# Kernel optimization log

Hardware: AMD Instinct MI355X
Metric: run time of the kernel (lower is better)

Reference implementation:

```python
import jax, jax.numpy as jnp
import numpy as np

K = 5            # dimW
PARAM_SIGMA = 0.08
LAMBDA_V = 2.0
C_MID = 192


def _conv5(x, w, b):
    # standard 5x5 SAME conv (the linear 'm' term of INRF)
    y = jax.lax.conv_general_dilated(x, w, (1, 1), 'SAME',
                                     dimension_numbers=('NCHW', 'OIHW', 'NCHW'))
    return y + b[None, :, None, None]


def _inrf(x, m_w, m_b, w_w):
    """INRF layer: out = (m * x) - lambda * sum_y w(y) sigma(x(y) - (g*x)(center)).
    dimG=1 so the Gaussian g*x is the identity (center pixel). The radiometric
    nonlinearity sigma is a saturating tanh with slope 1/paramSigma.
    """
    B, C, H, W = x.shape
    # windowed gather: [B, C*K*K, H, W], channel-major / spatial-minor ordering
    patches = jax.lax.conv_general_dilated_patches(x, (K, K), (1, 1), 'SAME')
    patches = patches.reshape(B, C, K * K, H, W)
    s = jnp.tanh((patches - x[:, :, None]) / PARAM_SIGMA)   # [B,C,KK,H,W]
    wterm = jnp.einsum('bckhw,ock->bohw', s, w_w)           # [B,Cout,H,W]
    return _conv5(x, m_w, m_b) - LAMBDA_V * wterm


def _maxpool2(x):
    return jax.lax.reduce_window(x, -jnp.inf, jax.lax.max,
                                 (1, 1, 2, 2), (1, 1, 2, 2), 'VALID')


def _avgpool8(x):
    s = jax.lax.reduce_window(x, 0.0, jax.lax.add,
                              (1, 1, 8, 8), (1, 1, 8, 8), 'VALID')
    return s / 64.0


def setup_inputs() -> dict:
    key = jax.random.key(0)
    ks = jax.random.split(key, 11)
    B = 64
    f32 = jnp.float32
    return {
        'x':    jax.random.normal(ks[0], (B, 3, 32, 32), f32),
        'm1_w': jax.random.normal(ks[1], (C_MID, 3, K, K), f32) * 0.05,
        'm1_b': jnp.zeros((C_MID,), f32),
        'w1_w': jax.random.normal(ks[2], (C_MID, 3, K * K), f32) * 0.05,
        'm2_w': jax.random.normal(ks[3], (C_MID, C_MID, K, K), f32) * 0.02,
        'm2_b': jnp.zeros((C_MID,), f32),
        'w2_w': jax.random.normal(ks[4], (C_MID, C_MID, K * K), f32) * 0.02,
        'm3_w': jax.random.normal(ks[5], (C_MID, C_MID, K, K), f32) * 0.02,
        'm3_b': jnp.zeros((C_MID,), f32),
        'w3_w': jax.random.normal(ks[6], (C_MID, C_MID, K * K), f32) * 0.02,
        'fc_w': jax.random.normal(ks[7], (10, C_MID), f32) * 0.05,
        'fc_b': jnp.zeros((10,), f32),
    }


def reference(x, m1_w, m1_b, w1_w, m2_w, m2_b, w2_w,
              m3_w, m3_b, w3_w, fc_w, fc_b):
    # dropout layers run in eval mode (identity); dp2d1 has p=0.0 anyway
    x00 = _maxpool2(_inrf(x, m1_w, m1_b, w1_w))      # [B,192,16,16]
    x01 = _inrf(x00, m2_w, m2_b, w2_w)               # [B,192,16,16]
    x03 = _maxpool2(x01)                             # [B,192,8,8]
    x04 = _inrf(x03, m3_w, m3_b, w3_w)               # [B,192,8,8]
    x05 = _avgpool8(x04)                             # [B,192,1,1]
    feat = x05.reshape(-1, C_MID)
    logits = feat @ fc_w.T + fc_b                    # [B,10]
    return (logits, x00, x01)
```

## Files before the change

kernel.cpp:

```cpp
#include <hip/hip_runtime.h>
#include <math.h>

#define COUT 192
#define NF 12

typedef __bf16 bf16_8 __attribute__((ext_vector_type(8)));
typedef float  f32x4  __attribute__((ext_vector_type(4)));

__device__ __forceinline__ float fast_tanh125(float d) {
    float e = __builtin_amdgcn_exp2f(d * 36.06737602222409f);
    return 1.0f - 2.0f * __builtin_amdgcn_rcpf(e + 1.0f);
}

__device__ __forceinline__ void gl_lds16(const void* gptr, void* lptr) {
    auto g = (const __attribute__((address_space(1))) unsigned int*)gptr;
    auto l = (__attribute__((address_space(3))) unsigned int*)lptr;
    __builtin_amdgcn_global_load_lds(g, l, 16, 0, 0);
}

__global__ void prep_all(const float* __restrict__ m1_w, const float* __restrict__ w1_w,
                         const float* __restrict__ m2_w, const float* __restrict__ w2_w,
                         const float* __restrict__ m3_w, const float* __restrict__ w3_w,
                         __bf16* __restrict__ Bp1, __bf16* __restrict__ Bp2,
                         __bf16* __restrict__ Bp3, float* __restrict__ x00p) {
    int idx = blockIdx.x * 256 + threadIdx.x;
    const int N1 = 3 * 2 * NF * 64, N2 = 192 * 2 * NF * 64;
    const int NW = N1 + 2 * N2;
    if (idx >= NW) {
        int zi = idx - NW;
        if (zi < 1228800) ((f32x4*)x00p)[zi] = (f32x4){0.f, 0.f, 0.f, 0.f};
        return;
    }
    const float *mw, *ww; __bf16* Bp; int CIN, li;
    if (idx < N1)           { mw = m1_w; ww = w1_w; Bp = Bp1; CIN = 3;   li = idx; }
    else if (idx < N1 + N2) { mw = m2_w; ww = w2_w; Bp = Bp2; CIN = 192; li = idx - N1; }
    else                    { mw = m3_w; ww = w3_w; Bp = Bp3; CIN = 192; li = idx - N1 - N2; }
    int lane = li & 63;
    int nf = (li >> 6) % NF;
    int cc = li / (NF * 64);
    int t = cc & 1, c = cc >> 1;
    int n = nf * 16 + (lane & 15);
    int k0 = (lane >> 4) * 8;
    bf16_8 v;
    #pragma unroll
    for (int e = 0; e < 8; ++e) {
        int k = k0 + e;
        float val = 0.f;
        if (k < 25) {
            val = (t == 0) ? mw[((size_t)n * CIN + c) * 25 + k]
                           : -2.0f * ww[((size_t)n * CIN + c) * 25 + k];
        }
        v[e] = (__bf16)val;
    }
    *(bf16_8*)(Bp + (size_t)li * 8) = v;
}

__global__ __launch_bounds__(256, 3) void inrf1_mfma(
    const float* __restrict__ x, const __bf16* __restrict__ Bp,
    const float* __restrict__ bias, float* __restrict__ x00,
    float* __restrict__ x00p)
{
    __shared__ float win[3][6][36];
    __shared__ float hp[192][33];

    const int b  = blockIdx.x >> 4;
    const int h0 = (blockIdx.x & 15) * 2;
    const int tid = threadIdx.x;
    const int wv = tid >> 6, lane = tid & 63;
    const int hl = wv >> 1, half = wv & 1;
    const int mcol = lane & 15, q = lane >> 4;
    const int wpos = half * 16 + mcol;

    for (int i = tid; i < 3 * 6 * 36; i += 256) {
        int c = i / 216, r = (i / 36) % 6, cc = i % 36;
        int gr = h0 + r - 2, gc = cc - 2;
        float v = 0.f;
        if (gr >= 0 && gr < 32 && gc >= 0 && gc < 32)
            v = x[((size_t)(b * 3 + c) * 32 + gr) * 32 + gc];
        win[c][r][cc] = v;
    }
    __syncthreads();

    int offs[8];
    #pragma unroll
    for (int e = 0; e < 8; ++e) {
        int k = q * 8 + e;
        int kk = (k < 25) ? k : 0;
        offs[e] = (hl + kk / 5) * 36 + wpos + (kk % 5);
    }
    const int cen_off = (hl + 2) * 36 + wpos + 2;

    f32x4 acc[NF];
    #pragma unroll
    for (int j = 0; j < NF; ++j) acc[j] = (f32x4){0.f, 0.f, 0.f, 0.f};

    const float* winf = &win[0][0][0];
    for (int c = 0; c < 3; ++c) {
        const float* wf = winf + c * 216;
        float cen = wf[cen_off];
        bf16_8 av, as_;
        #pragma unroll
        for (int e = 0; e < 8; ++e) {
            float v = wf[offs[e]];
            av[e] = (__bf16)v;
            as_[e] = (__bf16)fast_tanh125(v - cen);
        }
        const bf16_8* b0 = (const bf16_8*)Bp + ((size_t)(c * 2 + 0) * NF) * 64 + lane;
        const bf16_8* b1 = b0 + NF * 64;
        #pragma unroll
        for (int j = 0; j < NF; ++j)
            acc[j] = __builtin_amdgcn_mfma_f32_16x16x32_bf16(av, b0[j * 64], acc[j], 0, 0, 0);
        #pragma unroll
        for (int j = 0; j < NF; ++j)
            acc[j] = __builtin_amdgcn_mfma_f32_16x16x32_bf16(as_, b1[j * 64], acc[j], 0, 0, 0);
    }

    #pragma unroll
    for (int j = 0; j < NF; ++j) {
        int n = j * 16 + mcol;
        hp[n][hl * 16 + half * 8 + q * 2 + 0] = fmaxf(acc[j][0], acc[j][1]);
        hp[n][hl * 16 + half * 8 + q * 2 + 1] = fmaxf(acc[j][2], acc[j][3]);
    }
    __syncthreads();

    const int hpout = h0 >> 1;
    for (int i = tid; i < 192 * 16; i += 256) {
        int n = i >> 4, wp = i & 15;
        float v = fmaxf(hp[n][wp], hp[n][16 + wp]) + bias[n];
        x00[((size_t)(b * COUT + n) * 16 + hpout) * 16 + wp] = v;
        x00p[(size_t)(b * COUT + n) * 400 + (hpout + 2) * 20 + (wp + 2)] = v;
    }
}

__global__ __launch_bounds__(512, 2) void inrf2_mfma(
    const float* __restrict__ x00p, const __bf16* __restrict__ Bp,
    float* __restrict__ out0, float* __restrict__ part)
{
    constexpr int CPS = 48;
    __shared__ __align__(16) __bf16 Bs[3][24 * 64 * 8];

    const int b  = blockIdx.x >> 2;
    const int ks = blockIdx.x & 3;
    const int c0 = ks * CPS;
    const int tid = threadIdx.x;
    const int wv = tid >> 6, lane = tid & 63;
    const int mg = wv & 3, nh = wv >> 2;
    const int wp = lane & 15, q = lane >> 4;

    int goff[9];
    #pragma unroll
    for (int e = 0; e < 8; ++e) {
        int kk = q * 8 + e;
        int k2 = (kk < 25) ? kk : 12;
        int dy = k2 / 5 - 2, dx = k2 % 5 - 2;
        goff[e] = (mg * 4 + dy + 2) * 20 + (wp + dx + 2);
    }
    goff[8] = (mg * 4 + 2) * 20 + (wp + 2);

    const float* xs = x00p + (size_t)(b * COUT + c0) * 400;

    f32x4 acc[4][6];
    #pragma unroll
    for (int m = 0; m < 4; ++m)
        #pragma unroll
        for (int j = 0; j < 6; ++j) acc[m][j] = (f32x4){0.f, 0.f, 0.f, 0.f};

#define ISSUE_B(c, slot)                                                   \
    {                                                                      \
        const __bf16* gB = Bp + (size_t)(c) * 12288 + wv * 1536 + lane * 8;\
        _Pragma("unroll")                                                  \
        for (int i = 0; i < 3; ++i)                                        \
            gl_lds16(gB + i * 512, &Bs[(slot)][wv * 1536 + i * 512]);      \
    }

#define LOAD_A(c, DST)                                                     \
    {                                                                      \
        const float* xc = xs + (size_t)(c) * 400;                          \
        _Pragma("unroll")                                                  \
        for (int m = 0; m < 4; ++m) {                                      \
            _Pragma("unroll")                                              \
            for (int i = 0; i < 9; ++i)                                    \
                (DST)[m][i] = xc[goff[i] + m * 20];                        \
        }                                                                  \
    }

#define STEP(r, CUR, NXT)                                                  \
    {                                                                      \
        const int sl_cur = (r) % 3;                                        \
        if ((r) + 2 < CPS) ISSUE_B(c0 + (r) + 2, ((r) + 2) % 3);           \
        if ((r) + 1 < CPS) LOAD_A((r) + 1, NXT);                           \
        bf16_8 av[4], as_[4];                                              \
        _Pragma("unroll")                                                  \
        for (int m = 0; m < 4; ++m) {                                      \
            float cen = (CUR)[m][8];                                       \
            _Pragma("unroll")                                              \
            for (int e = 0; e < 8; ++e) {                                  \
                float v = (CUR)[m][e];                                     \
                av[m][e] = (__bf16)v;                                      \
                as_[m][e] = (__bf16)fast_tanh125(v - cen);                 \
            }                                                              \
        }                                                                  \
        const bf16_8* Bf = (const bf16_8*)(Bs[sl_cur]) + lane;             \
        _Pragma("unroll")                                                  \
        for (int j = 0; j < 6; ++j) {                                      \
            bf16_8 fm = Bf[(nh * 6 + j) * 64];                             \
            bf16_8 fs = Bf[(12 + nh * 6 + j) * 64];                        \
            _Pragma("unroll")                                              \
            for (int m = 0; m < 4; ++m) {                                  \
                acc[m][j] = __builtin_amdgcn_mfma_f32_16x16x32_bf16(av[m],  fm, acc[m][j], 0, 0, 0); \
                acc[m][j] = __builtin_amdgcn_mfma_f32_16x16x32_bf16(as_[m], fs, acc[m][j], 0, 0, 0); \
            }                                                              \
        }                                                                  \
        __builtin_amdgcn_s_barrier();                                      \
    }

    float arawA[4][9], arawB[4][9];

    ISSUE_B(c0, 0);
    asm volatile("s_waitcnt vmcnt(0)" ::: "memory");
    __builtin_amdgcn_s_barrier();
    ISSUE_B(c0 + 1, 1);
    LOAD_A(0, arawA);

    for (int r2 = 0; r2 < CPS / 2; ++r2) {
        STEP(2 * r2,     arawA, arawB);
        STEP(2 * r2 + 1, arawB, arawA);
    }
#undef STEP
#undef LOAD_A
#undef ISSUE_B

    float* outp = (ks == 0) ? out0 : (part + (size_t)(ks - 1) * 3145728);
    #pragma unroll
    for (int j = 0; j < 6; ++j) {
        int n = (nh * 6 + j) * 16 + wp;
        #pragma unroll
        for (int m = 0; m < 4; ++m) {
            int h = mg * 4 + m;
            *(f32x4*)&outp[((size_t)(b * COUT + n)) * 256 + h * 16 + q * 4] = acc[m][j];
        }
    }
}

__global__ __launch_bounds__(512) void finish2(
    float* __restrict__ x01, const float* __restrict__ part,
    const float* __restrict__ bias, __bf16* __restrict__ An)
{
    __shared__ float xbuf[8][256];
    const int b  = blockIdx.x / 24;
    const int cg = blockIdx.x % 24;
    const int tid = threadIdx.x;
    const int wv = tid >> 6, lane = tid & 63;
    const int ch = cg * 8 + wv;

    float* p0 = x01 + ((size_t)b * COUT + ch) * 256;
    const float* pp = part + ((size_t)b * COUT + ch) * 256;
    const float bv = bias[ch];
    #pragma unroll
    for (int i = 0; i < 4; ++i) {
        int idx = lane + 64 * i;
        float s = ((p0[idx] + pp[idx]) + pp[idx + 3145728]) + pp[idx + 2 * 3145728] + bv;
        xbuf[wv][idx] = s;
        p0[idx] = s;
    }
    __syncthreads();

    const int ph = lane >> 3, pw = lane & 7;
    const int i0 = ph * 32 + pw * 2;
    float x8 = fmaxf(fmaxf(xbuf[wv][i0], xbuf[wv][i0 + 1]),
                     fmaxf(xbuf[wv][i0 + 16], xbuf[wv][i0 + 17]));

    float myT = 0.f, myW = 0.f;
    #pragma unroll
    for (int k = 0; k < 25; ++k) {
        const int dy = k / 5 - 2, dx = k % 5 - 2;
        const bool valid = (ph + dy >= 0) && (ph + dy < 8) && (pw + dx >= 0) && (pw + dx < 8);
        float nb = __shfl(x8, (lane + dy * 8 + dx) & 63);
        nb = valid ? nb : 0.f;
        float tS = fast_tanh125(nb - x8);
        float wS = nb;
        #pragma unroll
        for (int off = 1; off < 64; off <<= 1) {
            tS += __shfl_xor(tS, off);
            wS += __shfl_xor(wS, off);
        }
        if (lane == k) { myT = tS; myW = wS; }
    }

    const int mt = b >> 4;
    if (lane < 25) {
        const int k = lane;
        const int la = (k >> 3) * 16 + (b & 15);
        const int e = k & 7;
        const int ccW = ch * 2, ccT = ch * 2 + 1;
        An[((size_t)(ccW * 4 + mt) * 64 + la) * 8 + e] = (__bf16)(myW * 0.015625f);
        An[((size_t)(ccT * 4 + mt) * 64 + la) * 8 + e] = (__bf16)(myT * 0.015625f);
    } else if (lane < 32) {
        const int la = 3 * 16 + (b & 15);
        const int e = lane & 7;
        const int ccW = ch * 2, ccT = ch * 2 + 1;
        An[((size_t)(ccW * 4 + mt) * 64 + la) * 8 + e] = (__bf16)0.f;
        An[((size_t)(ccT * 4 + mt) * 64 + la) * 8 + e] = (__bf16)0.f;
    }
}

__global__ __launch_bounds__(512) void gemm3p(
    const __bf16* __restrict__ An, const __bf16* __restrict__ Bp,
    float* __restrict__ part)
{
    const int ks = blockIdx.x;
    const int tid = threadIdx.x;
    const int wv = tid >> 6, lane = tid & 63;
    const int mt = wv & 3, nh = wv >> 2;

    f32x4 acc[6];
    #pragma unroll
    for (int j = 0; j < 6; ++j) acc[j] = (f32x4){0.f, 0.f, 0.f, 0.f};

    for (int i = 0; i < 4; ++i) {
        const int cc = ks * 4 + i;
        bf16_8 a = *(const bf16_8*)(An + ((size_t)(cc * 4 + mt) * 64 + lane) * 8);
        #pragma unroll
        for (int j = 0; j < 6; ++j) {
            bf16_8 bw = *(const bf16_8*)(Bp + ((size_t)(cc * NF + nh * 6 + j) * 64 + lane) * 8);
            acc[j] = __builtin_amdgcn_mfma_f32_16x16x32_bf16(a, bw, acc[j], 0, 0, 0);
        }
    }
    #pragma unroll
    for (int j = 0; j < 6; ++j) {
        int n = (nh * 6 + j) * 16 + (lane & 15);
        *(f32x4*)(part + ((size_t)ks * COUT + n) * 64 + mt * 16 + (lane >> 4) * 4) = acc[j];
    }
}

__global__ __launch_bounds__(256) void logitsk(
    const float* __restrict__ part, const float* __restrict__ m3_b,
    const float* __restrict__ fc_w, const float* __restrict__ fc_b,
    float* __restrict__ logits)
{
    __shared__ float feat[COUT];
    const int b = blockIdx.x;
    const int t = threadIdx.x;
    if (t < COUT) {
        float s = 0.f;
        for (int ks = 0; ks < 96; ++ks) s += part[((size_t)ks * COUT + t) * 64 + b];
        feat[t] = s + m3_b[t];
    }
    __syncthreads();
    if (t < 10) {
        float s = fc_b[t];
        #pragma unroll 8
        for (int c = 0; c < COUT; ++c) s = fmaf(fc_w[t * COUT + c], feat[c], s);
        logits[(size_t)b * 10 + t] = s;
    }
}

extern "C" void kernel_launch(void* const* d_in, const int* in_sizes, int n_in,
                              void* d_out, int out_size, void* d_ws, size_t ws_size,
                              hipStream_t stream) {
    const float* x    = (const float*)d_in[0];
    const float* m1_w = (const float*)d_in[1];
    const float* m1_b = (const float*)d_in[2];
    const float* w1_w = (const float*)d_in[3];
    const float* m2_w = (const float*)d_in[4];
    const float* m2_b = (const float*)d_in[5];
    const float* w2_w = (const float*)d_in[6];
    const float* m3_w = (const float*)d_in[7];
    const float* m3_b = (const float*)d_in[8];
    const float* w3_w = (const float*)d_in[9];
    const float* fc_w = (const float*)d_in[10];
    const float* fc_b = (const float*)d_in[11];

    float* out = (float*)d_out;
    float* ws  = (float*)d_ws;

    float* logits = out;
    float* x00 = out + 640;
    float* x01 = out + 640 + 3145728;

    __bf16* Bp1  = (__bf16*)(ws);
    __bf16* Bp2  = (__bf16*)(ws + 18432);
    __bf16* Bp3  = (__bf16*)(ws + 1198080);
    __bf16* An   = (__bf16*)(ws + 2377728);
    float*  part2 = ws + 2770944;
    float*  part3 = ws + 2770944;
    float*  x00p  = ws + 12208128;

    prep_all<<<7122, 256, 0, stream>>>(m1_w, w1_w, m2_w, w2_w, m3_w, w3_w,
                                       Bp1, Bp2, Bp3, x00p);

    inrf1_mfma<<<64 * 16, 256, 0, stream>>>(x, Bp1, m1_b, x00, x00p);
    inrf2_mfma<<<64 * 4, 512, 0, stream>>>(x00p, Bp2, x01, part2);
    finish2<<<64 * 24, 512, 0, stream>>>(x01, part2, m2_b, An);
    gemm3p<<<96, 512, 0, stream>>>(An, Bp3, part3);
    logitsk<<<64, 256, 0, stream>>>(part3, m3_b, fc_w, fc_b, logits);
}
```

Baseline: 231.0 us.

## Load inrf2 weights directly into registers and split output channels across blocks

The inrf2 kernel stops staging B weight fragments through LDS with global_load_lds and barriers. Each wave now loads its weight fragments straight into registers with double buffering, while the A-side patch loads move inline into each step. The grid doubles to 512 blocks of 256 threads, and each block covers half of the output channels, which removes the intra-block barrier. In exchange, weights are fetched redundantly by every wave with no LDS sharing, register pressure goes up, and the A loads are no longer prefetched.

```diff
diff --git a/kernel.cpp b/kernel.cpp
--- a/kernel.cpp
+++ b/kernel.cpp
@@ -10,12 +10,6 @@
 __device__ __forceinline__ float fast_tanh125(float d) {
     float e = __builtin_amdgcn_exp2f(d * 36.06737602222409f);
     return 1.0f - 2.0f * __builtin_amdgcn_rcpf(e + 1.0f);
-}
-
-__device__ __forceinline__ void gl_lds16(const void* gptr, void* lptr) {
-    auto g = (const __attribute__((address_space(1))) unsigned int*)gptr;
-    auto l = (__attribute__((address_space(3))) unsigned int*)lptr;
-    __builtin_amdgcn_global_load_lds(g, l, 16, 0, 0);
 }
 
 __global__ void prep_all(const float* __restrict__ m1_w, const float* __restrict__ w1_w,
@@ -132,19 +126,18 @@
     }
 }
 
-__global__ __launch_bounds__(512, 2) void inrf2_mfma(
+__global__ __launch_bounds__(256, 2) void inrf2_mfma(
     const float* __restrict__ x00p, const __bf16* __restrict__ Bp,
     float* __restrict__ out0, float* __restrict__ part)
 {
     constexpr int CPS = 48;
-    __shared__ __align__(16) __bf16 Bs[3][24 * 64 * 8];
-
-    const int b  = blockIdx.x >> 2;
-    const int ks = blockIdx.x & 3;
+    const int bid = blockIdx.x;
+    const int b  = bid >> 3;
+    const int ks = (bid >> 1) & 3;
+    const int nb = bid & 1;
     const int c0 = ks * CPS;
     const int tid = threadIdx.x;
     const int wv = tid >> 6, lane = tid & 63;
-    const int mg = wv & 3, nh = wv >> 2;
     const int wp = lane & 15, q = lane >> 4;
 
     int goff[9];
@@ -153,11 +146,12 @@
         int kk = q * 8 + e;
         int k2 = (kk < 25) ? kk : 12;
         int dy = k2 / 5 - 2, dx = k2 % 5 - 2;
-        goff[e] = (mg * 4 + dy + 2) * 20 + (wp + dx + 2);
-    }
-    goff[8] = (mg * 4 + 2) * 20 + (wp + 2);
+        goff[e] = (wv * 4 + dy + 2) * 20 + (wp + dx + 2);
+    }
+    goff[8] = (wv * 4 + 2) * 20 + (wp + 2);
 
     const float* xs = x00p + (size_t)(b * COUT + c0) * 400;
+    const __bf16* Bb = Bp + (size_t)c0 * 12288 + (size_t)nb * 6 * 512 + (size_t)lane * 8;
 
     f32x4 acc[4][6];
     #pragma unroll
@@ -165,78 +159,59 @@
         #pragma unroll
         for (int j = 0; j < 6; ++j) acc[m][j] = (f32x4){0.f, 0.f, 0.f, 0.f};
 
-#define ISSUE_B(c, slot)                                                   \
+#define LOAD_B(c, DST)                                                     \
     {                                                                      \
-        const __bf16* gB = Bp + (size_t)(c) * 12288 + wv * 1536 + lane * 8;\
+        const __bf16* gB = Bb + (size_t)(c) * 12288;                       \
         _Pragma("unroll")                                                  \
-        for (int i = 0; i < 3; ++i)                                        \
-            gl_lds16(gB + i * 512, &Bs[(slot)][wv * 1536 + i * 512]);      \
-    }
-
-#define LOAD_A(c, DST)                                                     \
+        for (int j = 0; j < 6; ++j) {                                      \
+            (DST)[j]     = *(const bf16_8*)(gB + j * 512);                 \
+            (DST)[6 + j] = *(const bf16_8*)(gB + 6144 + j * 512);          \
+        }                                                                  \
+    }
+
+#define STEP(r, CB, NB)                                                    \
     {                                                                      \
-        const float* xc = xs + (size_t)(c) * 400;                          \
-        _Pragma("unroll")                                                  \
-        for (int m = 0; m < 4; ++m) {                                      \
-            _Pragma("unroll")                                              \
-            for (int i = 0; i < 9; ++i)                                    \
-                (DST)[m][i] = xc[goff[i] + m * 20];                        \
-        }                                                                  \
-    }
-
-#define STEP(r, CUR, NXT)                                                  \
-    {                                                                      \
-        const int sl_cur = (r) % 3;                                        \
-        if ((r) + 2 < CPS) ISSUE_B(c0 + (r) + 2, ((r) + 2) % 3);           \
-        if ((r) + 1 < CPS) LOAD_A((r) + 1, NXT);                           \
+        if ((r) + 1 < CPS) LOAD_B((r) + 1, NB);                            \
+        const float* xc = xs + (size_t)(r) * 400;                          \
         bf16_8 av[4], as_[4];                                              \
         _Pragma("unroll")                                                  \
         for (int m = 0; m < 4; ++m) {                                      \
-            float cen = (CUR)[m][8];                                       \
+            float raw[9];                                                  \
+            _Pragma("unroll")                                              \
+            for (int i = 0; i < 9; ++i) raw[i] = xc[goff[i] + m * 20];     \
+            float cen = raw[8];                                            \
             _Pragma("unroll")                                              \
             for (int e = 0; e < 8; ++e) {                                  \
-                float v = (CUR)[m][e];                                     \
-                av[m][e] = (__bf16)v;                                      \
-                as_[m][e] = (__bf16)fast_tanh125(v - cen);                 \
+                av[m][e] = (__bf16)raw[e];                                 \
+                as_[m][e] = (__bf16)fast_tanh125(raw[e] - cen);            \
             }                                                              \
         }                                                                  \
-        const bf16_8* Bf = (const bf16_8*)(Bs[sl_cur]) + lane;             \
         _Pragma("unroll")                                                  \
         for (int j = 0; j < 6; ++j) {                                      \
-            bf16_8 fm = Bf[(nh * 6 + j) * 64];                             \
-            bf16_8 fs = Bf[(12 + nh * 6 + j) * 64];                        \
             _Pragma("unroll")                                              \
             for (int m = 0; m < 4; ++m) {                                  \
-                acc[m][j] = __builtin_amdgcn_mfma_f32_16x16x32_bf16(av[m],  fm, acc[m][j], 0, 0, 0); \
-                acc[m][j] = __builtin_amdgcn_mfma_f32_16x16x32_bf16(as_[m], fs, acc[m][j], 0, 0, 0); \
+                acc[m][j] = __builtin_amdgcn_mfma_f32_16x16x32_bf16(av[m],  (CB)[j],     acc[m][j], 0, 0, 0); \
+                acc[m][j] = __builtin_amdgcn_mfma_f32_16x16x32_bf16(as_[m], (CB)[6 + j], acc[m][j], 0, 0, 0); \
             }                                                              \
         }                                                                  \
-        __builtin_amdgcn_s_barrier();                                      \
-    }
-
-    float arawA[4][9], arawB[4][9];
-
-    ISSUE_B(c0, 0);
-    asm volatile("s_waitcnt vmcnt(0)" ::: "memory");
-    __builtin_amdgcn_s_barrier();
-    ISSUE_B(c0 + 1, 1);
-    LOAD_A(0, arawA);
-
+    }
+
+    bf16_8 bufA[12], bufB[12];
+    LOAD_B(0, bufA);
     for (int r2 = 0; r2 < CPS / 2; ++r2) {
-        STEP(2 * r2,     arawA, arawB);
-        STEP(2 * r2 + 1, arawB, arawA);
+        STEP(2 * r2,     bufA, bufB);
+        STEP(2 * r2 + 1, bufB, bufA);
     }
 #undef STEP
-#undef LOAD_A
-#undef ISSUE_B
+#undef LOAD_B
 
     float* outp = (ks == 0) ? out0 : (part + (size_t)(ks - 1) * 3145728);
     #pragma unroll
     for (int j = 0; j < 6; ++j) {
-        int n = (nh * 6 + j) * 16 + wp;
+        int n = (nb * 6 + j) * 16 + wp;
         #pragma unroll
         for (int m = 0; m < 4; ++m) {
-            int h = mg * 4 + m;
+            int h = wv * 4 + m;
             *(f32x4*)&outp[((size_t)(b * COUT + n)) * 256 + h * 16 + q * 4] = acc[m][j];
         }
     }
@@ -390,7 +365,7 @@
                                        Bp1, Bp2, Bp3, x00p);
 
     inrf1_mfma<<<64 * 16, 256, 0, stream>>>(x, Bp1, m1_b, x00, x00p);
-    inrf2_mfma<<<64 * 4, 512, 0, stream>>>(x00p, Bp2, x01, part2);
+    inrf2_mfma<<<64 * 8, 256, 0, stream>>>(x00p, Bp2, x01, part2);
     finish2<<<64 * 24, 512, 0, stream>>>(x01, part2, m2_b, An);
     gemm3p<<<96, 512, 0, stream>>>(An, Bp3, part3);
     logitsk<<<64, 256, 0, stream>>>(part3, m3_b, fc_w, fc_b, logits);
```

Result: faster. 213.3 us (-7.7%).
